# Optimization experiments

Hardware: AMD Instinct MI355X
Metric: run time of the kernel (lower is better)

The kernel has to match this reference:

```python
import jax, jax.numpy as jnp
import numpy as np

NUM_HEADS = 12
HEAD_DIM = 64
HIDDEN = NUM_HEADS * HEAD_DIM
AGENT_NUM = 40
MAX_POS = 2048
SCALE = HEAD_DIM ** -0.5


def _split_heads(x):
    # [b, s, hidden] -> [b, h, s, d]
    b, s, _ = x.shape
    return x.reshape(b, s, NUM_HEADS, HEAD_DIM).transpose(0, 2, 1, 3)


def _agent_pool(q, agent_num):
    # F.interpolate(q[None], size=(agent_num, dim), mode='bilinear', align_corners=False)
    # width (dim) is unchanged so it reduces to 1D linear interp along seq axis.
    b, s, dim = q.shape
    src = (jnp.arange(agent_num, dtype=q.dtype) + 0.5) * (s / agent_num) - 0.5
    src = jnp.clip(src, 0.0, s - 1.0)
    lo = jnp.floor(src).astype(jnp.int32)
    hi = jnp.minimum(lo + 1, s - 1)
    w = (src - lo.astype(q.dtype))[None, :, None]  # [1, A, 1]
    return q[:, lo, :] * (1.0 - w) + q[:, hi, :] * w  # [b, A, dim]


def setup_inputs() -> dict:
    key = jax.random.key(0)
    ks = jax.random.split(key, 6)
    bs, S = 16, 2048
    return {
        "hidden_states": jax.random.normal(ks[0], (bs, S, HIDDEN), jnp.float32),
        "attention_mask": jnp.zeros((bs, 1, 1, S), jnp.float32),
        "Wq": jax.random.normal(ks[1], (HIDDEN, HIDDEN), jnp.float32) * 0.02,
        "bq": jnp.zeros((HIDDEN,), jnp.float32),
        "Wk": jax.random.normal(ks[2], (HIDDEN, HIDDEN), jnp.float32) * 0.02,
        "bk": jnp.zeros((HIDDEN,), jnp.float32),
        "Wv": jax.random.normal(ks[3], (HIDDEN, HIDDEN), jnp.float32) * 0.02,
        "bv": jnp.zeros((HIDDEN,), jnp.float32),
        "dist_emb": jax.random.normal(ks[4], (2 * MAX_POS - 1, HEAD_DIM), jnp.float32) * 0.02,
    }


def reference(hidden_states, attention_mask, Wq, bq, Wk, bk, Wv, bv, dist_emb):
    bs, S, dim = hidden_states.shape
    q = hidden_states @ Wq + bq          # [b, S, hidden] (== query_layer flattened back)
    k = hidden_states @ Wk + bk
    v = hidden_states @ Wv + bv
    q_layer = _split_heads(q)            # [b, h, S, d]
    k_layer = _split_heads(k)
    v_layer = _split_heads(v)

    agent = _agent_pool(q, AGENT_NUM)    # [b, A, hidden]
    agent_layer = _split_heads(agent)    # [b, h, A, d]

    # stage 1: agent -> KV, with relative-key position bias
    d1 = jnp.arange(AGENT_NUM)[:, None] - jnp.arange(S)[None, :] + (MAX_POS - 1)
    pe1 = dist_emb[d1]                   # [A, S, d]
    bias1 = jnp.einsum('bhad,asd->bhas', agent_layer, pe1)
    score1 = jnp.einsum('bhad,bhsd->bhas', agent_layer * SCALE, k_layer) + bias1
    score1 = score1 + attention_mask     # [b,1,1,S] broadcasts over (h, A)
    p1 = jax.nn.softmax(score1, axis=-1)
    agent_v = jnp.einsum('bhas,bhsd->bhad', p1, v_layer)  # [b, h, A, d]

    # stage 2: query -> agents, with relative-key position bias
    d2 = jnp.arange(S)[:, None] - jnp.arange(AGENT_NUM)[None, :] + (MAX_POS - 1)
    pe2 = dist_emb[d2]                   # [S, A, d]
    bias2 = jnp.einsum('bhsd,sad->bhsa', q_layer, pe2)
    score2 = jnp.einsum('bhsd,bhad->bhsa', q_layer * SCALE, agent_layer) + bias2
    q_mask = jnp.swapaxes(attention_mask, -1, -2)  # [b,1,S,1]
    score2 = score2 + q_mask
    p2 = jax.nn.softmax(score2, axis=-1)
    x = jnp.einsum('bhsa,bhad->bhsd', p2, agent_v)  # [b, h, S, d]
    return x.transpose(0, 2, 1, 3).reshape(bs, S, dim)
```

## Files before the change

### kernel.cpp

```cpp
#include <hip/hip_runtime.h>
#include <math.h>

#define B_ 16
#define S_ 2048
#define H_ 12
#define D_ 64
#define HID 768
#define A_ 40
#define SCALE_ 0.125f
#define CH1 8
#define SUBT 64
#define NSUB 4

typedef __attribute__((ext_vector_type(8))) short short8v;
typedef __attribute__((ext_vector_type(4))) float f32x4;
typedef __attribute__((ext_vector_type(16))) float f32x16;

__device__ __forceinline__ unsigned f2bf_bits(float x) {
    unsigned u = __float_as_uint(x);
    return (u + 0x7FFFu + ((u >> 16) & 1u)) >> 16;
}

__device__ __forceinline__ void split1(float v, unsigned short& h, unsigned short& l) {
    __bf16 bh = (__bf16)v;
    float hf = (float)bh;
    __bf16 bl = (__bf16)(v - hf);
    h = __builtin_bit_cast(unsigned short, bh);
    l = __builtin_bit_cast(unsigned short, bl);
}

__device__ __forceinline__ void split8c(const float* x, int4& hi, int4& lo) {
    unsigned h[8], l[8];
#pragma unroll
    for (int i = 0; i < 8; i++) {
        __bf16 bh = (__bf16)x[i];
        float hf = (float)bh;
        __bf16 bl = (__bf16)(x[i] - hf);
        h[i] = (unsigned)__builtin_bit_cast(unsigned short, bh);
        l[i] = (unsigned)__builtin_bit_cast(unsigned short, bl);
    }
    hi = make_int4((int)(h[0] | (h[1] << 16)), (int)(h[2] | (h[3] << 16)),
                   (int)(h[4] | (h[5] << 16)), (int)(h[6] | (h[7] << 16)));
    lo = make_int4((int)(l[0] | (l[1] << 16)), (int)(l[2] | (l[3] << 16)),
                   (int)(l[4] | (l[5] << 16)), (int)(l[6] | (l[7] << 16)));
}

#define WT_BLKS 1728
#define DF_BLKS 128
#define D0_BLKS 66
__global__ __launch_bounds__(256) void preconvert(
    const float* __restrict__ Wq, const float* __restrict__ Wk, const float* __restrict__ Wv,
    const float* __restrict__ dist,
    unsigned short* __restrict__ Wth, unsigned short* __restrict__ Wtl,
    unsigned short* __restrict__ DFh, unsigned short* __restrict__ DFl,
    unsigned short* __restrict__ D0h, unsigned short* __restrict__ D0l)
{
    const int bx = blockIdx.x;
    const int t = threadIdx.x;
    if (bx < WT_BLKS) {
        int idx = bx * 256 + t;
        if (idx >= 3 * 192 * 768) return;
        int n  = idx % 768;
        int kc = (idx / 768) % 192;
        int z  = idx / (768 * 192);
        const float* W = (z == 0) ? Wq : (z == 1) ? Wk : Wv;
        unsigned short h4[4], l4[4];
#pragma unroll
        for (int i = 0; i < 4; i++) {
            float x = W[(size_t)(4 * kc + i) * HID + n];
            unsigned hb = f2bf_bits(x);
            float hf = __uint_as_float(hb << 16);
            h4[i] = (unsigned short)hb;
            l4[i] = (unsigned short)f2bf_bits(x - hf);
        }
        size_t o = ((size_t)z * HID + n) * HID + 4 * kc;
        *(ushort4*)&Wth[o] = make_ushort4(h4[0], h4[1], h4[2], h4[3]);
        *(ushort4*)&Wtl[o] = make_ushort4(l4[0], l4[1], l4[2], l4[3]);
    } else if (bx < WT_BLKS + DF_BLKS) {
        int g = (bx - WT_BLKS) * 256 + t;
        int lane = g & 63;
        int ks = (g >> 6) & 1;
        int u  = g >> 7;
        int row = 8 + u * 16 + (lane & 15);
        int col = ks * 32 + ((lane >> 4) << 3);
        float xv[8];
#pragma unroll
        for (int j = 0; j < 8; j++)
            xv[j] = (row < 4095) ? dist[(size_t)row * D_ + col + j] : 0.f;
        int4 hi, lo;
        split8c(xv, hi, lo);
        *(int4*)&DFh[(size_t)g * 8] = hi;
        *(int4*)&DFl[(size_t)g * 8] = lo;
    } else {
        int g = (bx - WT_BLKS - DF_BLKS) * 256 + t;
        if (g >= 131 * 2 * 64) return;
        int lane = g & 63;
        int ks = (g >> 6) & 1;
        int u  = g >> 7;
        int row = u * 16 + (lane & 15);
        int col = ks * 32 + ((lane >> 4) << 3);
        float xv[8];
#pragma unroll
        for (int j = 0; j < 8; j++) xv[j] = dist[(size_t)row * D_ + col + j];
        int4 hi, lo;
        split8c(xv, hi, lo);
        *(int4*)&D0h[(size_t)g * 8] = hi;
        *(int4*)&D0l[(size_t)g * 8] = lo;
    }
}

__global__ void avt_frag(const float* __restrict__ AgV,
                         unsigned short* __restrict__ Vh, unsigned short* __restrict__ Vl)
{
    int g = blockIdx.x * 256 + threadIdx.x;
    if (g >= 192 * 4 * 2 * 64) return;
    int lane = g & 63;
    int r = g >> 6;
    int ks = r & 1; r >>= 1;
    int nt = r & 3;
    int bh = r >> 2;
    int d = nt * 16 + (lane & 15);
    int a0 = ks * 32 + ((lane >> 4) << 3);
    float xv[8];
#pragma unroll
    for (int j = 0; j < 8; j++) {
        int a = a0 + j;
        xv[j] = (a < A_) ? AgV[((size_t)bh * A_ + a) * D_ + d] : 0.f;
    }
    int4 hi, lo;
    split8c(xv, hi, lo);
    *(int4*)&Vh[(size_t)g * 8] = hi;
    *(int4*)&Vl[(size_t)g * 8] = lo;
}

__global__ __launch_bounds__(512, 2) void qkv_z(
    const float* __restrict__ X,
    const unsigned short* __restrict__ Wth, const unsigned short* __restrict__ Wtl,
    const float* __restrict__ bq, const float* __restrict__ bk, const float* __restrict__ bv,
    float* __restrict__ Q, float* __restrict__ K, float* __restrict__ V)
{
    const int L   = blockIdx.x;
    const int k8  = L & 7, sl_ = L >> 3;
    const int mt  = k8 * 32 + sl_ / 9;
    const int sub = sl_ % 9;
    const int nt  = sub % 3, zz = sub / 3;
    const int m0 = mt * 128, n0 = nt * 256;

    const float* __restrict__ bias = (zz == 0) ? bq : (zz == 1) ? bk : bv;
    float* __restrict__ Out        = (zz == 0) ? Q  : (zz == 1) ? K  : V;
    const unsigned short* __restrict__ Bhg = Wth + (size_t)zz * HID * HID;
    const unsigned short* __restrict__ Blg = Wtl + (size_t)zz * HID * HID;

    __shared__ unsigned short Ah[128][40];
    __shared__ unsigned short Al[128][40];
    __shared__ unsigned short Bh[256][40];
    __shared__ unsigned short Bl[256][40];

    const int t = threadIdx.x;
    const int lane = t & 63, w = t >> 6;
    const int wm = (w & 1) * 64, wn = (w >> 1) * 64;
    const int r32 = lane & 31, kh = lane >> 5;

    const int sr = t >> 2, sca = (t & 3) * 8;
    const int sb = t >> 1, scb = (t & 1) * 16;

    f32x16 acc[2][2];
#pragma unroll
    for (int i = 0; i < 2; i++)
#pragma unroll
        for (int j = 0; j < 2; j++)
#pragma unroll
            for (int p = 0; p < 16; p++) acc[i][j][p] = 0.f;

    for (int k0 = 0; k0 < HID; k0 += 32) {
        float xv[8];
        const float* xp = X + (size_t)(m0 + sr) * HID + k0 + sca;
        float4 f0 = *(const float4*)xp;
        float4 f1 = *(const float4*)(xp + 4);
        xv[0] = f0.x; xv[1] = f0.y; xv[2] = f0.z; xv[3] = f0.w;
        xv[4] = f1.x; xv[5] = f1.y; xv[6] = f1.z; xv[7] = f1.w;
        int4 ah, al;
        split8c(xv, ah, al);
        size_t bo = (size_t)(n0 + sb) * HID + k0 + scb;
        int4 bh0 = *(const int4*)&Bhg[bo];
        int4 bh1 = *(const int4*)&Bhg[bo + 8];
        int4 bl0 = *(const int4*)&Blg[bo];
        int4 bl1 = *(const int4*)&Blg[bo + 8];

        __syncthreads();
        *(int4*)&Ah[sr][sca] = ah;
        *(int4*)&Al[sr][sca] = al;
        *(int4*)&Bh[sb][scb]     = bh0;  *(int4*)&Bh[sb][scb + 8] = bh1;
        *(int4*)&Bl[sb][scb]     = bl0;  *(int4*)&Bl[sb][scb + 8] = bl1;
        __syncthreads();

#pragma unroll
        for (int ks = 0; ks < 2; ks++) {
            const int ko = ks * 16 + kh * 8;
            short8v a_h[2], a_l[2], b_h[2], b_l[2];
#pragma unroll
            for (int i = 0; i < 2; i++) {
                a_h[i] = *(const short8v*)&Ah[wm + i * 32 + r32][ko];
                a_l[i] = *(const short8v*)&Al[wm + i * 32 + r32][ko];
                b_h[i] = *(const short8v*)&Bh[wn + i * 32 + r32][ko];
                b_l[i] = *(const short8v*)&Bl[wn + i * 32 + r32][ko];
            }
#pragma unroll
            for (int i = 0; i < 2; i++)
#pragma unroll
                for (int j = 0; j < 2; j++) {
                    acc[i][j] = __builtin_amdgcn_mfma_f32_32x32x16_bf16(a_h[i], b_h[j], acc[i][j], 0, 0, 0);
                    acc[i][j] = __builtin_amdgcn_mfma_f32_32x32x16_bf16(a_l[i], b_h[j], acc[i][j], 0, 0, 0);
                    acc[i][j] = __builtin_amdgcn_mfma_f32_32x32x16_bf16(a_h[i], b_l[j], acc[i][j], 0, 0, 0);
                }
        }
    }

    const float scl = (zz == 1) ? SCALE_ : 1.0f;
#pragma unroll
    for (int j = 0; j < 2; j++) {
        int n = n0 + wn + j * 32 + r32;
        float bj = bias[n];
        int h = n >> 6, d = n & 63;
#pragma unroll
        for (int i = 0; i < 2; i++) {
#pragma unroll
            for (int p = 0; p < 16; p++) {
                int m = m0 + wm + i * 32 + (p & 3) + 8 * (p >> 2) + 4 * kh;
                int b = m >> 11, s = m & 2047;
                Out[(((size_t)b * H_ + h) * S_ + s) * D_ + d] = (acc[i][j][p] + bj) * scl;
            }
        }
    }
}

__global__ __launch_bounds__(256) void agpool_frag(
    const float* __restrict__ Q,
    unsigned short* __restrict__ AGFh, unsigned short* __restrict__ AGFl,
    unsigned short* __restrict__ AG1h, unsigned short* __restrict__ AG1l)
{
    const int bh = blockIdx.x;
    const int t = threadIdx.x;
    __shared__ float ag[A_][D_];
    const float* base = Q + (size_t)bh * (S_ * D_);
    for (int i = t; i < A_ * D_; i += 256) {
        int d = i & 63, a = i >> 6;
        float src = ((float)a + 0.5f) * (2048.0f / 40.0f) - 0.5f;
        src = fminf(fmaxf(src, 0.0f), 2047.0f);
        int lo = (int)floorf(src);
        int hi = min(lo + 1, S_ - 1);
        float w = src - (float)lo;
        ag[a][d] = base[lo * D_ + d] * (1.0f - w) + base[hi * D_ + d] * w;
    }
    __syncthreads();
    for (int g = t; g < 384; g += 256) {
        int lane = g & 63;
        int ks = (g >> 6) & 1;
        int at = g >> 7;
        int a = at * 16 + (lane & 15);
        int col = ks * 32 + ((lane >> 4) << 3);
        float xs[8], x1[8];
#pragma unroll
        for (int j = 0; j < 8; j++) {
            float v = (a < A_) ? ag[a][col + j] : 0.f;
            x1[j] = v; xs[j] = v * SCALE_;
        }
        int4 h1, l1, h2, l2;
        split8c(xs, h1, l1);
        split8c(x1, h2, l2);
        size_t o = ((((size_t)bh * 3 + at) * 2 + ks) * 64 + lane) * 8;
        *(int4*)&AGFh[o] = h1;  *(int4*)&AGFl[o] = l1;
        *(int4*)&AG1h[o] = h2;  *(int4*)&AG1l[o] = l2;
    }
}

__global__ __launch_bounds__(256, 2) void stage1_mfma(
    const float* __restrict__ Kl, const float* __restrict__ Vl,
    const unsigned short* __restrict__ AG1h, const unsigned short* __restrict__ AG1l,
    const unsigned short* __restrict__ D0h,  const unsigned short* __restrict__ D0l,
    const float* __restrict__ mask,
    float* __restrict__ Pacc, float* __restrict__ Pm, float* __restrict__ Pl)
{
    const int q  = blockIdx.x;
    const int bh = blockIdx.y;
    const int b  = bh / H_;
    const int s0 = q * (NSUB * SUBT);
    const float* __restrict__ kb = Kl + (size_t)bh * (S_ * D_);
    const float* __restrict__ vb = Vl + (size_t)bh * (S_ * D_);

    __shared__ unsigned short KFh[4096], KFl[4096];
    __shared__ unsigned short VTh[4096], VTl[4096];
    __shared__ float sc[SUBT][52];
    __shared__ float scp[112][52];
    __shared__ float pm6[6][A_];
    __shared__ float mrow[A_], lrow[A_], resc[A_], mrw[SUBT];

    const int t = threadIdx.x;
    const int lane = t & 63, w = t >> 6;
    const int fr = lane & 15, kg = lane >> 4;

    if (t < A_) { mrow[t] = -INFINITY; lrow[t] = 0.0f; }

    f32x4 acc3[3];
#pragma unroll
    for (int at = 0; at < 3; at++) acc3[at] = (f32x4){0.f, 0.f, 0.f, 0.f};

    for (int st = 0; st < NSUB; st++) {
        const int sb = s0 + st * SUBT;
        const int u0 = (1984 - sb) >> 4;

        __syncthreads();

        {
            const int r = t >> 2, c0 = (t & 3) * 16;
            const float* kp = kb + (size_t)(sb + r) * D_ + c0;
            float xa[8], xb[8];
            float4 f0 = *(const float4*)(kp);
            float4 f1 = *(const float4*)(kp + 4);
            float4 f2 = *(const float4*)(kp + 8);
            float4 f3 = *(const float4*)(kp + 12);
            xa[0]=f0.x; xa[1]=f0.y; xa[2]=f0.z; xa[3]=f0.w;
            xa[4]=f1.x; xa[5]=f1.y; xa[6]=f1.z; xa[7]=f1.w;
            xb[0]=f2.x; xb[1]=f2.y; xb[2]=f2.z; xb[3]=f2.w;
            xb[4]=f3.x; xb[5]=f3.y; xb[6]=f3.z; xb[7]=f3.w;
            int4 h0, l0, h1, l1;
            split8c(xa, h0, l0);
            split8c(xb, h1, l1);
            const int tsr = r >> 4, frr = r & 15;
            const int c8a = (t & 3) * 2, c8b = c8a + 1;
            const int oa = ((tsr * 2 + (c8a >> 2)) * 64 + (((c8a & 3) << 4) | frr)) * 8;
            const int ob = ((tsr * 2 + (c8b >> 2)) * 64 + (((c8b & 3) << 4) | frr)) * 8;
            *(int4*)&KFh[oa] = h0;  *(int4*)&KFl[oa] = l0;
            *(int4*)&KFh[ob] = h1;  *(int4*)&KFl[ob] = l1;
        }
        {
            const int r = t >> 2, c0 = (t & 3) * 16;
            const float* vp = vb + (size_t)(sb + r) * D_ + c0;
            float vv[16];
            float4 g0 = *(const float4*)(vp);
            float4 g1 = *(const float4*)(vp + 4);
            float4 g2 = *(const float4*)(vp + 8);
            float4 g3 = *(const float4*)(vp + 12);
            vv[0]=g0.x; vv[1]=g0.y; vv[2]=g0.z; vv[3]=g0.w;
            vv[4]=g1.x; vv[5]=g1.y; vv[6]=g1.z; vv[7]=g1.w;
            vv[8]=g2.x; vv[9]=g2.y; vv[10]=g2.z; vv[11]=g2.w;
            vv[12]=g3.x; vv[13]=g3.y; vv[14]=g3.z; vv[15]=g3.w;
            const int ks2 = r >> 5, kgp = (r & 31) >> 3, e = r & 7;
#pragma unroll
            for (int jj = 0; jj < 16; jj++) {
                int d = c0 + jj;
                int off = (((d >> 4) * 2 + ks2) * 64 + kgp * 16 + (d & 15)) * 8 + e;
                unsigned short h, l;
                split1(vv[jj], h, l);
                VTh[off] = h; VTl[off] = l;
            }
        }
        if (t < SUBT) mrw[t] = mask[(size_t)b * S_ + sb + t];
        __syncthreads();

        {
            const int ts = w;
#pragma unroll
            for (int at = 0; at < 3; at++) {
                f32x4 a4 = (f32x4){0.f, 0.f, 0.f, 0.f};
#pragma unroll
                for (int ks = 0; ks < 2; ks++) {
                    size_t oA = ((((size_t)bh * 3 + at) * 2 + ks) * 64 + lane) * 8;
                    short8v gh = *(const short8v*)&AG1h[oA];
                    short8v gl = *(const short8v*)&AG1l[oA];
                    short8v kh2 = *(const short8v*)&KFh[((ts * 2 + ks) * 64 + lane) * 8];
                    short8v kl2 = *(const short8v*)&KFl[((ts * 2 + ks) * 64 + lane) * 8];
                    a4 = __builtin_amdgcn_mfma_f32_16x16x32_bf16(gh, kh2, a4, 0, 0, 0);
                    a4 = __builtin_amdgcn_mfma_f32_16x16x32_bf16(gl, kh2, a4, 0, 0, 0);
                    a4 = __builtin_amdgcn_mfma_f32_16x16x32_bf16(gh, kl2, a4, 0, 0, 0);
                }
                *(f32x4*)&sc[ts * 16 + fr][at * 16 + kg * 4] = a4;
            }
        }
        for (int ut = w; ut < 7; ut += 4) {
            const int u = u0 + ut;
#pragma unroll
            for (int at = 0; at < 3; at++) {
                f32x4 a4 = (f32x4){0.f, 0.f, 0.f, 0.f};
#pragma unroll
                for (int ks = 0; ks < 2; ks++) {
                    size_t oA = ((((size_t)bh * 3 + at) * 2 + ks) * 64 + lane) * 8;
                    short8v gh = *(const short8v*)&AG1h[oA];
                    short8v gl = *(const short8v*)&AG1l[oA];
                    size_t oD = (((size_t)u * 2 + ks) * 64 + lane) * 8;
                    short8v dh = *(const short8v*)&D0h[oD];
                    short8v dl = *(const short8v*)&D0l[oD];
                    a4 = __builtin_amdgcn_mfma_f32_16x16x32_bf16(gh, dh, a4, 0, 0, 0);
                    a4 = __builtin_amdgcn_mfma_f32_16x16x32_bf16(gl, dh, a4, 0, 0, 0);
                    a4 = __builtin_amdgcn_mfma_f32_16x16x32_bf16(gh, dl, a4, 0, 0, 0);
                }
                *(f32x4*)&scp[ut * 16 + fr][at * 16 + kg * 4] = a4;
            }
        }
        __syncthreads();

        for (int i = t; i < SUBT * A_; i += 256) {
            int rr = i / 40, aa = i - rr * 40;
            sc[rr][aa] += scp[aa + 63 - rr][aa] + mrw[rr];
        }
        __syncthreads();
        if (t < 240) {
            int a = t % 40, r6 = t / 40;
            float mx = -INFINITY;
            for (int i = r6; i < SUBT; i += 6) mx = fmaxf(mx, sc[i][a]);
            pm6[r6][a] = mx;
        }
        __syncthreads();
        if (t < A_) {
            float lm = pm6[0][t];
#pragma unroll
            for (int r6 = 1; r6 < 6; r6++) lm = fmaxf(lm, pm6[r6][t]);
            float mnew = fmaxf(mrow[t], lm);
            resc[t] = __expf(mrow[t] - mnew);
            mrow[t] = mnew;
        }
        __syncthreads();
        for (int i = t; i < SUBT * A_; i += 256) {
            int rr = i / 40, aa = i - rr * 40;
            sc[rr][aa] = __expf(sc[rr][aa] - mrow[aa]);
        }
        __syncthreads();
        if (t < 240) {
            int a = t % 40, r6 = t / 40;
            float sm = 0.0f;
            for (int i = r6; i < SUBT; i += 6) sm += sc[i][a];
            pm6[r6][a] = sm;
        }
        __syncthreads();
        if (t < A_) {
            float ls = pm6[0][t] + pm6[1][t] + pm6[2][t] + pm6[3][t] + pm6[4][t] + pm6[5][t];
            lrow[t] = lrow[t] * resc[t] + ls;
        }
        __syncthreads();

        for (int g = t; g < 384; g += 256) {
            int pl = g & 63;
            int c = g >> 6;
            int at = c >> 1, ks2 = c & 1;
            int a = at * 16 + (pl & 15);
            int sl0 = ks2 * 32 + (pl >> 4) * 8;
            float xv[8];
#pragma unroll
            for (int e = 0; e < 8; e++)
                xv[e] = (a < A_) ? sc[sl0 + e][a] : 0.f;
            int4 hi, lo;
            split8c(xv, hi, lo);
            *(int4*)&KFh[g * 8] = hi;
            *(int4*)&KFl[g * 8] = lo;
        }
        __syncthreads();

        {
            const int dt = w;
#pragma unroll
            for (int at = 0; at < 3; at++) {
                f32x4 a4 = acc3[at];
#pragma unroll
                for (int p = 0; p < 4; p++) {
                    int a = at * 16 + kg * 4 + p;
                    float rs = (a < A_) ? resc[a] : 0.f;
                    a4[p] *= rs;
                }
#pragma unroll
                for (int ks2 = 0; ks2 < 2; ks2++) {
                    short8v ph = *(const short8v*)&KFh[((at * 2 + ks2) * 64 + lane) * 8];
                    short8v pll = *(const short8v*)&KFl[((at * 2 + ks2) * 64 + lane) * 8];
                    short8v vh = *(const short8v*)&VTh[((dt * 2 + ks2) * 64 + lane) * 8];
                    short8v vl = *(const short8v*)&VTl[((dt * 2 + ks2) * 64 + lane) * 8];
                    a4 = __builtin_amdgcn_mfma_f32_16x16x32_bf16(ph, vh, a4, 0, 0, 0);
                    a4 = __builtin_amdgcn_mfma_f32_16x16x32_bf16(pll, vh, a4, 0, 0, 0);
                    a4 = __builtin_amdgcn_mfma_f32_16x16x32_bf16(ph, vl, a4, 0, 0, 0);
                }
                acc3[at] = a4;
            }
        }
    }
    __syncthreads();

    {
        const int dt = w;
#pragma unroll
        for (int at = 0; at < 3; at++) {
#pragma unroll
            for (int p = 0; p < 4; p++) {
                int a = at * 16 + kg * 4 + p;
                if (a < A_)
                    Pacc[(((size_t)(bh * CH1 + q) * A_) + a) * D_ + dt * 16 + fr] = acc3[at][p];
            }
        }
    }
    if (t < A_) {
        Pm[(size_t)(bh * CH1 + q) * A_ + t] = mrow[t];
        Pl[(size_t)(bh * CH1 + q) * A_ + t] = lrow[t];
    }
}

__global__ __launch_bounds__(256) void stage1_reduce(
    const float* __restrict__ Pacc, const float* __restrict__ Pm,
    const float* __restrict__ Pl, float* __restrict__ AgV)
{
    const int bh = blockIdx.x;
    const int t = threadIdx.x;
    __shared__ float F[CH1][A_], Linv[A_];
    if (t < A_) {
        float M = -INFINITY;
#pragma unroll
        for (int q = 0; q < CH1; q++) M = fmaxf(M, Pm[(size_t)(bh * CH1 + q) * A_ + t]);
        float L = 0.0f;
#pragma unroll
        for (int q = 0; q < CH1; q++) {
            float f = __expf(Pm[(size_t)(bh * CH1 + q) * A_ + t] - M);
            F[q][t] = f;
            L = fmaf(f, Pl[(size_t)(bh * CH1 + q) * A_ + t], L);
        }
        Linv[t] = 1.0f / L;
    }
    __syncthreads();
#pragma unroll
    for (int ii = 0; ii < 3; ii++) {
        int i = t + ii * 256;
        if (i < A_ * 16) {
            int a = i >> 4, d4 = i & 15;
            float4 s4 = make_float4(0.f, 0.f, 0.f, 0.f);
            for (int q = 0; q < CH1; q++) {
                float f = F[q][a];
                float4 p4 = *(const float4*)&Pacc[(((size_t)(bh * CH1 + q) * A_) + a) * D_ + d4 * 4];
                s4.x = fmaf(f, p4.x, s4.x);
                s4.y = fmaf(f, p4.y, s4.y);
                s4.z = fmaf(f, p4.z, s4.z);
                s4.w = fmaf(f, p4.w, s4.w);
            }
            float inv = Linv[a];
            s4.x *= inv; s4.y *= inv; s4.z *= inv; s4.w *= inv;
            *(float4*)&AgV[(size_t)bh * (A_ * D_) + a * D_ + d4 * 4] = s4;
        }
    }
}

__global__ __launch_bounds__(256, 3) void stage2_mfma(
    const float* __restrict__ Qg,
    const unsigned short* __restrict__ AGFh, const unsigned short* __restrict__ AGFl,
    const unsigned short* __restrict__ DFh,  const unsigned short* __restrict__ DFl,
    const unsigned short* __restrict__ AVFh, const unsigned short* __restrict__ AVFl,
    float* __restrict__ Out)
{
    const int sb8 = blockIdx.x;
    const int bh  = blockIdx.y;
    const int b = bh / H_, h = bh % H_;

    __shared__ float scm[64][52];
    __shared__ float scp[64][68];
    __shared__ unsigned short PAh[64][72], PAl[64][72];

    const int t = threadIdx.x;
    const int lane = t & 63, ts = t >> 6;
    const int fr = lane & 15, kg = lane >> 4;

    short8v agh[3][2], agl[3][2];
#pragma unroll
    for (int at = 0; at < 3; at++)
#pragma unroll
        for (int ks = 0; ks < 2; ks++) {
            size_t o = ((((size_t)bh * 3 + at) * 2 + ks) * 64 + lane) * 8;
            agh[at][ks] = *(const short8v*)&AGFh[o];
            agl[at][ks] = *(const short8v*)&AGFl[o];
        }

    const float* qlane = Qg + ((size_t)bh * S_ + sb8 * 256 + ts * 16 + fr) * D_ + kg * 8;

    float4 f0 = *(const float4*)(qlane);
    float4 f1 = *(const float4*)(qlane + 4);
    float4 f2 = *(const float4*)(qlane + 32);
    float4 f3 = *(const float4*)(qlane + 36);

    for (int c = 0; c < 4; c++) {
        const int s0 = sb8 * 256 + c * 64;
        const int base_u = (s0 >> 4) + 125;

        float xa[8] = {f0.x, f0.y, f0.z, f0.w, f1.x, f1.y, f1.z, f1.w};
        float xb[8] = {f2.x, f2.y, f2.z, f2.w, f3.x, f3.y, f3.z, f3.w};
        int4 h0, l0, h1, l1;
        split8c(xa, h0, l0);
        split8c(xb, h1, l1);
        short8v qh[2], ql[2];
        qh[0] = __builtin_bit_cast(short8v, h0);  ql[0] = __builtin_bit_cast(short8v, l0);
        qh[1] = __builtin_bit_cast(short8v, h1);  ql[1] = __builtin_bit_cast(short8v, l1);

        if (c < 3) {
            const float* np = qlane + (size_t)(c + 1) * 64 * D_;
            f0 = *(const float4*)(np);
            f1 = *(const float4*)(np + 4);
            f2 = *(const float4*)(np + 32);
            f3 = *(const float4*)(np + 36);
        }

#pragma unroll
        for (int at = 0; at < 3; at++) {
            f32x4 acc = (f32x4){0.f, 0.f, 0.f, 0.f};
#pragma unroll
            for (int ks = 0; ks < 2; ks++) {
                acc = __builtin_amdgcn_mfma_f32_16x16x32_bf16(agh[at][ks], qh[ks], acc, 0, 0, 0);
                acc = __builtin_amdgcn_mfma_f32_16x16x32_bf16(agl[at][ks], qh[ks], acc, 0, 0, 0);
                acc = __builtin_amdgcn_mfma_f32_16x16x32_bf16(agh[at][ks], ql[ks], acc, 0, 0, 0);
            }
            *(f32x4*)&scm[ts * 16 + fr][at * 16 + kg * 4] = acc;
        }
#pragma unroll
        for (int o4 = 0; o4 < 4; o4++) {
            f32x4 acc = (f32x4){0.f, 0.f, 0.f, 0.f};
            const int u = base_u + ts + o4;
#pragma unroll
            for (int ks = 0; ks < 2; ks++) {
                size_t o = (((size_t)u * 2 + ks) * 64 + lane) * 8;
                short8v chv = *(const short8v*)&DFh[o];
                short8v clv = *(const short8v*)&DFl[o];
                acc = __builtin_amdgcn_mfma_f32_16x16x32_bf16(chv, qh[ks], acc, 0, 0, 0);
                acc = __builtin_amdgcn_mfma_f32_16x16x32_bf16(clv, qh[ks], acc, 0, 0, 0);
                acc = __builtin_amdgcn_mfma_f32_16x16x32_bf16(chv, ql[ks], acc, 0, 0, 0);
            }
            *(f32x4*)&scp[ts * 16 + fr][o4 * 16 + kg * 4] = acc;
        }
        __syncthreads();

        {
            const int rr = t >> 2, dq = t & 3;
            const int base = (rr & 15) + 39;
            float val[10];
#pragma unroll
            for (int i = 0; i < 10; i++) {
                int a = dq * 10 + i;
                val[i] = scm[rr][a] + scp[rr][base - a];
            }
            float mx = -INFINITY;
#pragma unroll
            for (int i = 0; i < 10; i++) mx = fmaxf(mx, val[i]);
            mx = fmaxf(mx, __shfl_xor(mx, 1));
            mx = fmaxf(mx, __shfl_xor(mx, 2));
            float sum = 0.f;
#pragma unroll
            for (int i = 0; i < 10; i++) { val[i] = __expf(val[i] - mx); sum += val[i]; }
            sum += __shfl_xor(sum, 1);
            sum += __shfl_xor(sum, 2);
            float inv = 1.0f / sum;
            unsigned* ph = (unsigned*)&PAh[rr][0];
            unsigned* pl = (unsigned*)&PAl[rr][0];
#pragma unroll
            for (int i = 0; i < 5; i++) {
                unsigned short hh0, ll0, hh1, ll1;
                split1(val[2 * i] * inv, hh0, ll0);
                split1(val[2 * i + 1] * inv, hh1, ll1);
                ph[dq * 5 + i] = (unsigned)hh0 | ((unsigned)hh1 << 16);
                pl[dq * 5 + i] = (unsigned)ll0 | ((unsigned)ll1 << 16);
            }
#pragma unroll
            for (int i = 0; i < 3; i++) { ph[20 + dq * 3 + i] = 0u; pl[20 + dq * 3 + i] = 0u; }
        }
        __syncthreads();

        short8v ph8[2], pl8[2];
#pragma unroll
        for (int ks = 0; ks < 2; ks++) {
            ph8[ks] = *(const short8v*)&PAh[ts * 16 + fr][ks * 32 + kg * 8];
            pl8[ks] = *(const short8v*)&PAl[ts * 16 + fr][ks * 32 + kg * 8];
        }
#pragma unroll
        for (int nt = 0; nt < 4; nt++) {
            f32x4 acc = (f32x4){0.f, 0.f, 0.f, 0.f};
#pragma unroll
            for (int ks = 0; ks < 2; ks++) {
                size_t o = ((((size_t)bh * 4 + nt) * 2 + ks) * 64 + lane) * 8;
                short8v vh = *(const short8v*)&AVFh[o];
                short8v vl = *(const short8v*)&AVFl[o];
                acc = __builtin_amdgcn_mfma_f32_16x16x32_bf16(ph8[ks], vh, acc, 0, 0, 0);
                acc = __builtin_amdgcn_mfma_f32_16x16x32_bf16(pl8[ks], vh, acc, 0, 0, 0);
                acc = __builtin_amdgcn_mfma_f32_16x16x32_bf16(ph8[ks], vl, acc, 0, 0, 0);
            }
            const int d = nt * 16 + fr;
            float* op = Out + ((size_t)b * S_ + s0 + ts * 16 + kg * 4) * HID + h * D_ + d;
#pragma unroll
            for (int rr = 0; rr < 4; rr++)
                op[(size_t)rr * HID] = acc[rr];
        }
    }
}

extern "C" void kernel_launch(void* const* d_in, const int* in_sizes, int n_in,
                              void* d_out, int out_size, void* d_ws, size_t ws_size,
                              hipStream_t stream) {
    const float* hs   = (const float*)d_in[0];
    const float* mask = (const float*)d_in[1];
    const float* Wq   = (const float*)d_in[2];
    const float* bq   = (const float*)d_in[3];
    const float* Wk   = (const float*)d_in[4];
    const float* bk   = (const float*)d_in[5];
    const float* Wv   = (const float*)d_in[6];
    const float* bv   = (const float*)d_in[7];
    const float* dist = (const float*)d_in[8];
    float* out = (float*)d_out;

    float* ws = (float*)d_ws;
    const size_t QKV = (size_t)B_ * H_ * S_ * D_;
    const size_t AG  = (size_t)B_ * H_ * A_ * D_;
    float* Q     = ws;
    float* K     = ws + QKV;
    float* V     = ws + 2 * QKV;
    float* Agent = ws + 3 * QKV;
    float* AgV   = Agent + AG;
    float* Pacc  = AgV + AG;
    float* Pm    = Pacc + (size_t)B_ * H_ * CH1 * A_ * D_;
    float* Pl    = Pm + (size_t)B_ * H_ * CH1 * A_;
    unsigned short* Wth = (unsigned short*)(Pl + (size_t)B_ * H_ * CH1 * A_);
    unsigned short* Wtl = Wth + (size_t)3 * HID * HID;
    unsigned short* DFh = Wtl + (size_t)3 * HID * HID;
    unsigned short* DFl = DFh + (size_t)262144;
    unsigned short* AGFh = DFl + (size_t)262144;
    unsigned short* AGFl = AGFh + (size_t)589824;
    unsigned short* AVFh = AGFl + (size_t)589824;
    unsigned short* AVFl = AVFh + (size_t)786432;
    unsigned short* AG1h = AVFl + (size_t)786432;
    unsigned short* AG1l = AG1h + (size_t)589824;
    unsigned short* D0h  = AG1l + (size_t)589824;
    unsigned short* D0l  = D0h + (size_t)134144;

    preconvert<<<WT_BLKS + DF_BLKS + D0_BLKS, 256, 0, stream>>>(
        Wq, Wk, Wv, dist, Wth, Wtl, DFh, DFl, D0h, D0l);
    qkv_z<<<2304, 512, 0, stream>>>(hs, Wth, Wtl, bq, bk, bv, Q, K, V);
    agpool_frag<<<B_ * H_, 256, 0, stream>>>(Q, AGFh, AGFl, AG1h, AG1l);
    dim3 g1(CH1, B_ * H_);
    stage1_mfma<<<g1, 256, 0, stream>>>(K, V, AG1h, AG1l, D0h, D0l, mask, Pacc, Pm, Pl);
    stage1_reduce<<<B_ * H_, 256, 0, stream>>>(Pacc, Pm, Pl, AgV);
    avt_frag<<<(192 * 4 * 2 * 64 + 255) / 256, 256, 0, stream>>>(AgV, AVFh, AVFl);
    dim3 g2(8, B_ * H_);
    stage2_mfma<<<g2, 256, 0, stream>>>(Q, AGFh, AGFl, DFh, DFl, AVFh, AVFl, out);
}
```

Baseline: 582.8 us.

## Stage Q tile through shared memory with coalesced loads in stage2

Q rows are now loaded by each thread as 64 contiguous bytes (one row quarter), converted to bf16 hi/lo pairs, and written into an MFMA-fragment layout in shared memory. Waves then read their fragments from LDS, and the next chunk's conversion overlaps the softmax phase. Previously each lane fetched strided pieces straight into registers. The aim is better global coalescing. The cost is an extra LDS buffer, an extra barrier per chunk, and occupancy lowered from 3 to 2 blocks in the launch bounds.

```diff
diff --git a/kernel.cpp b/kernel.cpp
--- a/kernel.cpp
+++ b/kernel.cpp
@@ -542,7 +542,7 @@
     }
 }
 
-__global__ __launch_bounds__(256, 3) void stage2_mfma(
+__global__ __launch_bounds__(256, 2) void stage2_mfma(
     const float* __restrict__ Qg,
     const unsigned short* __restrict__ AGFh, const unsigned short* __restrict__ AGFl,
     const unsigned short* __restrict__ DFh,  const unsigned short* __restrict__ DFl,
@@ -553,6 +553,7 @@
     const int bh  = blockIdx.y;
     const int b = bh / H_, h = bh % H_;
 
+    __shared__ unsigned short Qfh[8 * 64 * 8], Qfl[8 * 64 * 8];
     __shared__ float scm[64][52];
     __shared__ float scp[64][68];
     __shared__ unsigned short PAh[64][72], PAl[64][72];
@@ -571,32 +572,45 @@
             agl[at][ks] = *(const short8v*)&AGFl[o];
         }
 
-    const float* qlane = Qg + ((size_t)bh * S_ + sb8 * 256 + ts * 16 + fr) * D_ + kg * 8;
-
-    float4 f0 = *(const float4*)(qlane);
-    float4 f1 = *(const float4*)(qlane + 4);
-    float4 f2 = *(const float4*)(qlane + 32);
-    float4 f3 = *(const float4*)(qlane + 36);
-
-    for (int c = 0; c < 4; c++) {
-        const int s0 = sb8 * 256 + c * 64;
-        const int base_u = (s0 >> 4) + 125;
-
+    const int r = t >> 2, c0 = (t & 3) * 16;
+    const int tsr = r >> 4, frr = r & 15;
+    const int c8a = (t & 3) * 2, c8b = c8a + 1;
+    const int oa = ((tsr * 2 + (c8a >> 2)) * 64 + (((c8a & 3) << 4) | frr)) * 8;
+    const int ob = ((tsr * 2 + (c8b >> 2)) * 64 + (((c8b & 3) << 4) | frr)) * 8;
+    const float* qbase = Qg + ((size_t)bh * S_ + sb8 * 256 + r) * D_ + c0;
+
+    {
+        float4 f0 = *(const float4*)(qbase);
+        float4 f1 = *(const float4*)(qbase + 4);
+        float4 f2 = *(const float4*)(qbase + 8);
+        float4 f3 = *(const float4*)(qbase + 12);
         float xa[8] = {f0.x, f0.y, f0.z, f0.w, f1.x, f1.y, f1.z, f1.w};
         float xb[8] = {f2.x, f2.y, f2.z, f2.w, f3.x, f3.y, f3.z, f3.w};
         int4 h0, l0, h1, l1;
         split8c(xa, h0, l0);
         split8c(xb, h1, l1);
+        *(int4*)&Qfh[oa] = h0;  *(int4*)&Qfl[oa] = l0;
+        *(int4*)&Qfh[ob] = h1;  *(int4*)&Qfl[ob] = l1;
+    }
+    __syncthreads();
+
+    for (int c = 0; c < 4; c++) {
+        const int s0 = sb8 * 256 + c * 64;
+        const int base_u = (s0 >> 4) + 125;
+
         short8v qh[2], ql[2];
-        qh[0] = __builtin_bit_cast(short8v, h0);  ql[0] = __builtin_bit_cast(short8v, l0);
-        qh[1] = __builtin_bit_cast(short8v, h1);  ql[1] = __builtin_bit_cast(short8v, l1);
-
+#pragma unroll
+        for (int ks = 0; ks < 2; ks++) {
+            qh[ks] = *(const short8v*)&Qfh[((ts * 2 + ks) * 64 + lane) * 8];
+            ql[ks] = *(const short8v*)&Qfl[((ts * 2 + ks) * 64 + lane) * 8];
+        }
+        float4 nf0, nf1, nf2, nf3;
         if (c < 3) {
-            const float* np = qlane + (size_t)(c + 1) * 64 * D_;
-            f0 = *(const float4*)(np);
-            f1 = *(const float4*)(np + 4);
-            f2 = *(const float4*)(np + 32);
-            f3 = *(const float4*)(np + 36);
+            const float* np = qbase + (size_t)(c + 1) * 64 * D_;
+            nf0 = *(const float4*)(np);
+            nf1 = *(const float4*)(np + 4);
+            nf2 = *(const float4*)(np + 8);
+            nf3 = *(const float4*)(np + 12);
         }
 
 #pragma unroll
@@ -627,6 +641,15 @@
         }
         __syncthreads();
 
+        if (c < 3) {
+            float xa[8] = {nf0.x, nf0.y, nf0.z, nf0.w, nf1.x, nf1.y, nf1.z, nf1.w};
+            float xb[8] = {nf2.x, nf2.y, nf2.z, nf2.w, nf3.x, nf3.y, nf3.z, nf3.w};
+            int4 h0, l0, h1, l1;
+            split8c(xa, h0, l0);
+            split8c(xb, h1, l1);
+            *(int4*)&Qfh[oa] = h0;  *(int4*)&Qfl[oa] = l0;
+            *(int4*)&Qfh[ob] = h1;  *(int4*)&Qfl[ob] = l1;
+        }
         {
             const int rr = t >> 2, dq = t & 3;
             const int base = (rr & 15) + 39;
@@ -686,6 +709,7 @@
             for (int rr = 0; rr < 4; rr++)
                 op[(size_t)rr * HID] = acc[rr];
         }
+        __syncthreads();
     }
 }
 
```

Measured after the change: 558.1 us. -4.2%, faster.
